# Performance work log

Hardware: AMD Instinct MI355X
Metric: run time of the kernel (lower is better)

## Reference

```python
import jax, jax.numpy as jnp
import numpy as np

B, E, T = 8192, 512, 32


def setup_inputs() -> dict:
    key = jax.random.key(0)
    k1, k2, k3, k4, k5, k6 = jax.random.split(key, 6)
    s1 = 1.0 / np.sqrt(E)  # torch nn.Linear default init scale (uniform bound)
    return {
        "g_exp": jax.random.normal(k1, (B, E), dtype=jnp.float32),
        "tissue_vector": jax.random.randint(k2, (B, 1), 0, T, dtype=jnp.int64),
        # per-tissue head params: Linear(E,E) then Linear(E,1)
        "W1": jax.random.uniform(k3, (T, E, E), jnp.float32, -s1, s1),
        "b1": jax.random.uniform(k4, (T, E), jnp.float32, -s1, s1),
        "W2": jax.random.uniform(k5, (T, E), jnp.float32, -s1, s1),
        "b2": jax.random.uniform(k6, (T,), jnp.float32, -s1, s1),
    }


def reference(g_exp, tissue_vector, W1, b1, W2, b2):
    # Each sample b is routed through the MLP head of its tissue id.
    # Vectorized: run every sample through every tissue head, then select.
    # h[b,t,:] = GELU(g_exp[b] @ W1[t] + b1[t])
    h = jax.nn.gelu(jnp.einsum("be,teh->bth", g_exp, W1) + b1[None, :, :],
                    approximate=False)  # exact erf GELU, matches torch nn.GELU
    # y[b,t] = softplus(h[b,t] @ W2[t] + b2[t])   (Softplus since loss_fn='poisson')
    y = jax.nn.softplus(jnp.einsum("bth,th->bt", h, W2) + b2[None, :])
    tid = tissue_vector[:, 0]  # [B], tissue id per sample
    return jnp.take_along_axis(y, tid[:, None], axis=1)  # [B, 1]
```

## Files before the change

### kernel.cpp

```cpp
#include <hip/hip_runtime.h>
#include <math.h>

#define B_N 8192
#define E_N 512
#define T_N 32
#define LDA 40

typedef short bf16x8 __attribute__((ext_vector_type(8)));
typedef float f32x4 __attribute__((ext_vector_type(4)));

#define WS_OFFS   256
#define WS_RANK   512
#define WS_ORDER  33280
#define WS_YACC   66048
#define WS_ASORT  98816
#define WS_W1T    8487424
#define WS_REQ    25264640

static __device__ __forceinline__ unsigned short f2bf(float f) {
    unsigned int u = __float_as_uint(f);
    unsigned int r = u + 0x7fffu + ((u >> 16) & 1u);
    return (unsigned short)(r >> 16);
}

__global__ __launch_bounds__(1024) void k_prep(
    const int* __restrict__ tv, int* __restrict__ offs_g,
    int* __restrict__ rank, int* __restrict__ order, float* __restrict__ yacc) {
    __shared__ int lh[16 * 32];
    __shared__ int wcur[16 * 32];
    __shared__ int offs_s[33];
    int tid = threadIdx.x;
    int w = tid >> 6;
    if (tid < 512) { lh[tid] = 0; }
    __syncthreads();
    int tval[8];
#pragma unroll
    for (int c = 0; c < 8; ++c) tval[c] = tv[c * 1024 + tid];
#pragma unroll
    for (int c = 0; c < 8; ++c) atomicAdd(&lh[w * 32 + tval[c]], 1);
    __syncthreads();
    if (tid < 32) {
        int s = 0;
#pragma unroll
        for (int ww = 0; ww < 16; ++ww) s += lh[ww * 32 + tid];
        int excl = 0;
#pragma unroll
        for (int i = 0; i < 32; ++i) {
            int v = __shfl(s, i, 64);
            if (i < tid) excl += v;
        }
        offs_s[tid] = excl;
        offs_g[tid] = excl;
        if (tid == 31) { offs_s[32] = excl + s; offs_g[32] = excl + s; }
    }
    __syncthreads();
    if (tid < 512) {
        int ww = tid >> 5, t = tid & 31;
        int s = offs_s[t];
        for (int w2 = 0; w2 < ww; ++w2) s += lh[w2 * 32 + t];
        wcur[ww * 32 + t] = s;
    }
    __syncthreads();
#pragma unroll
    for (int c = 0; c < 8; ++c) {
        int b = c * 1024 + tid;
        int pos = atomicAdd(&wcur[w * 32 + tval[c]], 1);
        rank[b] = pos;
        order[pos] = b;
    }
#pragma unroll
    for (int c = 0; c < 8; ++c) yacc[c * 1024 + tid] = 0.f;
}

__global__ __launch_bounds__(256) void k_convert(
    const float* __restrict__ W1, unsigned short* __restrict__ W1T,
    const float* __restrict__ g_exp, const int* __restrict__ rank,
    unsigned short* __restrict__ Asort) {
    int cid = blockIdx.x;
    int tid = threadIdx.x;
    if (cid < 2048) {
        __shared__ float T[64][65];
        int t = cid >> 6, r = cid & 63;
        int k0 = (r >> 3) * 64, n0 = (r & 7) * 64;
        int g = tid >> 4, c = tid & 15;
#pragma unroll
        for (int p = 0; p < 4; ++p) {
            int row = p * 16 + g;
            float4 v = *(const float4*)(W1 + ((size_t)t * E_N + k0 + row) * E_N + n0 + c * 4);
            T[c * 4 + 0][row] = v.x;
            T[c * 4 + 1][row] = v.y;
            T[c * 4 + 2][row] = v.z;
            T[c * 4 + 3][row] = v.w;
        }
        __syncthreads();
#pragma unroll
        for (int p = 0; p < 4; ++p) {
            int n = p * 16 + g;
            ushort4 o;
            o.x = f2bf(T[n][c * 4 + 0]);
            o.y = f2bf(T[n][c * 4 + 1]);
            o.z = f2bf(T[n][c * 4 + 2]);
            o.w = f2bf(T[n][c * 4 + 3]);
            *(ushort4*)(W1T + ((size_t)t * E_N + n0 + n) * E_N + k0 + c * 4) = o;
        }
    } else {
        int b0 = (cid - 2048) * 32;
#pragma unroll 4
        for (int pp = 0; pp < 16; ++pp) {
            int idx = pp * 256 + tid;
            int row = idx >> 7, c = idx & 127;
            int b = b0 + row;
            float4 v = *(const float4*)(g_exp + (size_t)b * E_N + c * 4);
            ushort4 o;
            o.x = f2bf(v.x); o.y = f2bf(v.y); o.z = f2bf(v.z); o.w = f2bf(v.w);
            *(ushort4*)(Asort + (size_t)rank[b] * E_N + c * 4) = o;
        }
    }
}

__global__ __launch_bounds__(256) void k_gemm_mfma(
    const unsigned short* __restrict__ Asort, const unsigned short* __restrict__ W1T,
    const float* __restrict__ b1, const float* __restrict__ W2,
    const int* __restrict__ offs, float* __restrict__ yacc) {
    int wi = blockIdx.x;
    int mt = wi >> 7;
    int rem = wi & 127;
    int t = rem >> 2, nt = rem & 3;
    int base = offs[t];
    int n_t = offs[t + 1] - base;
    int m0 = mt * 128;
    if (m0 >= n_t) return;
    int n0 = nt * 128;

    __shared__ __align__(16) unsigned short As[2][128 * LDA];
    __shared__ __align__(16) unsigned short Bs[2][128 * LDA];

    int tid = threadIdx.x;
    int wave = tid >> 6, lane = tid & 63;
    int quad = lane >> 4, l15 = lane & 15;
    int wm = (wave >> 1) * 64, wn = (wave & 1) * 64;

    int s_row0 = tid >> 2, s_c = tid & 3;
    int s_row1 = s_row0 + 64;
    int gr0 = base + m0 + s_row0; if (gr0 > B_N - 1) gr0 = B_N - 1;
    int gr1 = base + m0 + s_row1; if (gr1 > B_N - 1) gr1 = B_N - 1;
    const unsigned short* Bsrc = W1T + ((size_t)t * E_N + n0) * E_N;
    const unsigned short* a0p = Asort + (size_t)gr0 * E_N + s_c * 8;
    const unsigned short* a1p = Asort + (size_t)gr1 * E_N + s_c * 8;
    const unsigned short* b0p = Bsrc + (size_t)s_row0 * E_N + s_c * 8;
    const unsigned short* b1p = Bsrc + (size_t)s_row1 * E_N + s_c * 8;

    f32x4 acc[4][4];
#pragma unroll
    for (int mi = 0; mi < 4; ++mi)
#pragma unroll
        for (int ni = 0; ni < 4; ++ni) acc[mi][ni] = (f32x4){0.f, 0.f, 0.f, 0.f};

    int4 ar0, ar1, br0, br1;
    ar0 = *(const int4*)(a0p); ar1 = *(const int4*)(a1p);
    br0 = *(const int4*)(b0p); br1 = *(const int4*)(b1p);

    int buf = 0;
    for (int k0 = 0; k0 < E_N; k0 += 32) {
        *(int4*)(&As[buf][s_row0 * LDA + s_c * 8]) = ar0;
        *(int4*)(&As[buf][s_row1 * LDA + s_c * 8]) = ar1;
        *(int4*)(&Bs[buf][s_row0 * LDA + s_c * 8]) = br0;
        *(int4*)(&Bs[buf][s_row1 * LDA + s_c * 8]) = br1;
        if (k0 + 32 < E_N) {
            int koff = k0 + 32;
            ar0 = *(const int4*)(a0p + koff);
            ar1 = *(const int4*)(a1p + koff);
            br0 = *(const int4*)(b0p + koff);
            br1 = *(const int4*)(b1p + koff);
        }
        __syncthreads();
        bf16x8 af[4], bfr[4];
#pragma unroll
        for (int i = 0; i < 4; ++i) {
            af[i]  = *(const bf16x8*)(&As[buf][(wm + i * 16 + l15) * LDA + quad * 8]);
            bfr[i] = *(const bf16x8*)(&Bs[buf][(wn + i * 16 + l15) * LDA + quad * 8]);
        }
#pragma unroll
        for (int mi = 0; mi < 4; ++mi)
#pragma unroll
            for (int ni = 0; ni < 4; ++ni)
                acc[mi][ni] = __builtin_amdgcn_mfma_f32_16x16x32_bf16(
                    af[mi], bfr[ni], acc[mi][ni], 0, 0, 0);
        buf ^= 1;
    }

    float pr[4][4];
#pragma unroll
    for (int mi = 0; mi < 4; ++mi)
#pragma unroll
        for (int r = 0; r < 4; ++r) pr[mi][r] = 0.f;
#pragma unroll
    for (int ni = 0; ni < 4; ++ni) {
        int n = n0 + wn + ni * 16 + l15;
        float bb = b1[t * E_N + n];
        float w2 = W2[t * E_N + n];
#pragma unroll
        for (int mi = 0; mi < 4; ++mi)
#pragma unroll
            for (int r = 0; r < 4; ++r) {
                float u = acc[mi][ni][r] + bb;
                float gg = 0.5f * u * (1.f + erff(u * 0.70710678118654752f));
                pr[mi][r] = fmaf(gg, w2, pr[mi][r]);
            }
    }
#pragma unroll
    for (int off = 1; off <= 8; off <<= 1)
#pragma unroll
        for (int mi = 0; mi < 4; ++mi)
#pragma unroll
            for (int r = 0; r < 4; ++r) pr[mi][r] += __shfl_xor(pr[mi][r], off, 64);

    if (l15 == 0) {
#pragma unroll
        for (int mi = 0; mi < 4; ++mi)
#pragma unroll
            for (int r = 0; r < 4; ++r) {
                int row = m0 + wm + mi * 16 + quad * 4 + r;
                if (row < n_t) atomicAdd(&yacc[base + row], pr[mi][r]);
            }
    }
}

__global__ void k_final(const float* __restrict__ yacc, const int* __restrict__ rank,
                        const int* __restrict__ tv, const float* __restrict__ b2,
                        float* __restrict__ out, int use_rank) {
    int b = blockIdx.x * blockDim.x + threadIdx.x;
    if (b < B_N) {
        int idx = use_rank ? rank[b] : b;
        float x = yacc[idx] + b2[tv[b]];
        out[b] = fmaxf(x, 0.f) + log1pf(expf(-fabsf(x)));
    }
}

__global__ __launch_bounds__(256) void fb_gemm(
    const float* __restrict__ g_exp, const float* __restrict__ W1,
    const float* __restrict__ b1, const float* __restrict__ W2,
    const int* __restrict__ offs, const int* __restrict__ order,
    float* __restrict__ yacc) {
    int t = blockIdx.z;
    int base = offs[t];
    int n_t = offs[t + 1] - base;
    int m0 = blockIdx.y * 64;
    if (m0 >= n_t) return;
    int n0 = blockIdx.x * 128;

    __shared__ float As[32][68];
    __shared__ float Bs[32][128];
    __shared__ int sidx[64];

    int tid = threadIdx.x;
    if (tid < 64) {
        int m = m0 + tid;
        sidx[tid] = (m < n_t) ? order[base + m] : -1;
    }
    __syncthreads();

    int ty = tid >> 4, tx = tid & 15;
    float acc[4][8];
#pragma unroll
    for (int r = 0; r < 4; ++r)
#pragma unroll
        for (int c = 0; c < 8; ++c) acc[r][c] = 0.f;

    for (int k0 = 0; k0 < E_N; k0 += 32) {
#pragma unroll
        for (int p = 0; p < 2; ++p) {
            int idx = tid + 256 * p;
            int row = idx >> 3, kc = idx & 7;
            int s = sidx[row];
            float4 v = make_float4(0.f, 0.f, 0.f, 0.f);
            if (s >= 0) v = *(const float4*)(g_exp + (size_t)s * E_N + k0 + kc * 4);
            As[kc * 4 + 0][row] = v.x;
            As[kc * 4 + 1][row] = v.y;
            As[kc * 4 + 2][row] = v.z;
            As[kc * 4 + 3][row] = v.w;
        }
#pragma unroll
        for (int p = 0; p < 4; ++p) {
            int idx = tid + 256 * p;
            int kr = idx >> 5, c4 = idx & 31;
            *(float4*)(&Bs[kr][c4 * 4]) =
                *(const float4*)(W1 + ((size_t)t * E_N + (k0 + kr)) * E_N + n0 + c4 * 4);
        }
        __syncthreads();
#pragma unroll
        for (int e = 0; e < 32; ++e) {
            float4 a = *(const float4*)(&As[e][ty * 4]);
            float4 bA = *(const float4*)(&Bs[e][tx * 4]);
            float4 bB = *(const float4*)(&Bs[e][tx * 4 + 64]);
            float av[4] = {a.x, a.y, a.z, a.w};
            float bv[8] = {bA.x, bA.y, bA.z, bA.w, bB.x, bB.y, bB.z, bB.w};
#pragma unroll
            for (int r = 0; r < 4; ++r)
#pragma unroll
                for (int c = 0; c < 8; ++c) acc[r][c] = fmaf(av[r], bv[c], acc[r][c]);
        }
        __syncthreads();
    }

    float pr[4] = {0.f, 0.f, 0.f, 0.f};
#pragma unroll
    for (int c = 0; c < 8; ++c) {
        int n = n0 + tx * 4 + ((c >= 4) ? 64 : 0) + (c & 3);
        float bb = b1[t * E_N + n];
        float w2 = W2[t * E_N + n];
#pragma unroll
        for (int r = 0; r < 4; ++r) {
            float u = acc[r][c] + bb;
            float g = 0.5f * u * (1.f + erff(u * 0.70710678118654752f));
            pr[r] = fmaf(g, w2, pr[r]);
        }
    }
#pragma unroll
    for (int off = 8; off >= 1; off >>= 1)
#pragma unroll
        for (int r = 0; r < 4; ++r) pr[r] += __shfl_xor(pr[r], off, 64);

    if (tx == 0) {
#pragma unroll
        for (int r = 0; r < 4; ++r) {
            int m = m0 + ty * 4 + r;
            if (m < n_t) atomicAdd(&yacc[sidx[ty * 4 + r]], pr[r]);
        }
    }
}

extern "C" void kernel_launch(void* const* d_in, const int* in_sizes, int n_in,
                              void* d_out, int out_size, void* d_ws, size_t ws_size,
                              hipStream_t stream) {
    const float* g_exp = (const float*)d_in[0];
    const int*   tv    = (const int*)d_in[1];
    const float* W1    = (const float*)d_in[2];
    const float* b1    = (const float*)d_in[3];
    const float* W2    = (const float*)d_in[4];
    const float* b2    = (const float*)d_in[5];
    float* out = (float*)d_out;

    char* ws = (char*)d_ws;
    int* offs   = (int*)(ws + WS_OFFS);
    int* rank   = (int*)(ws + WS_RANK);
    int* order  = (int*)(ws + WS_ORDER);
    float* yacc = (float*)(ws + WS_YACC);

    if (ws_size >= (size_t)WS_REQ) {
        unsigned short* Asort = (unsigned short*)(ws + WS_ASORT);
        unsigned short* W1T   = (unsigned short*)(ws + WS_W1T);
        k_prep<<<1, 1024, 0, stream>>>(tv, offs, rank, order, yacc);
        k_convert<<<2304, 256, 0, stream>>>(W1, W1T, g_exp, rank, Asort);
        k_gemm_mfma<<<512, 256, 0, stream>>>(Asort, W1T, b1, W2, offs, yacc);
        k_final<<<32, 256, 0, stream>>>(yacc, rank, tv, b2, out, 1);
    } else {
        k_prep<<<1, 1024, 0, stream>>>(tv, offs, rank, order, yacc);
        fb_gemm<<<dim3(4, 8, 32), 256, 0, stream>>>(g_exp, W1, b1, W2, offs, order, yacc);
        k_final<<<32, 256, 0, stream>>>(yacc, rank, tv, b2, out, 0);
    }
}
```

Baseline: 137.2 us.

## Fuse tissue sort into W1 conversion and gather fp32 activations inside GEMM

The sort/histogram kernel is merged into the W1 transpose-convert kernel as one extra block, and the separate sorted bf16 activation buffer is removed. The GEMM now gathers fp32 rows of g_exp through the order array and converts them to bf16 in registers before writing to LDS. The B tile is loaded with global_load_lds direct-to-LDS copies using an unpadded stride. This removes one launch and one activation round trip through memory, at the cost of a single-block sort running alongside the conversion, possible LDS bank conflicts on the unpadded B tile, and conversion work inside the GEMM loop.

Result: slower. 144.8 us (+5.5%).

```diff
diff --git a/kernel.cpp b/kernel.cpp
--- a/kernel.cpp
+++ b/kernel.cpp
@@ -5,6 +5,7 @@
 #define E_N 512
 #define T_N 32
 #define LDA 40
+#define LDB 32
 
 typedef short bf16x8 __attribute__((ext_vector_type(8)));
 typedef float f32x4 __attribute__((ext_vector_type(4)));
@@ -13,71 +14,26 @@
 #define WS_RANK   512
 #define WS_ORDER  33280
 #define WS_YACC   66048
-#define WS_ASORT  98816
-#define WS_W1T    8487424
-#define WS_REQ    25264640
+#define WS_W1T    98816
+#define WS_REQ    (WS_W1T + (size_t)T_N * E_N * E_N * 2)
+
+typedef __attribute__((address_space(1))) const unsigned int gas_u32;
+typedef __attribute__((address_space(3))) unsigned int las_u32;
 
 static __device__ __forceinline__ unsigned short f2bf(float f) {
     unsigned int u = __float_as_uint(f);
     unsigned int r = u + 0x7fffu + ((u >> 16) & 1u);
     return (unsigned short)(r >> 16);
 }
-
-__global__ __launch_bounds__(1024) void k_prep(
+static __device__ __forceinline__ unsigned int pack2(float a, float b) {
+    return (unsigned int)f2bf(a) | ((unsigned int)f2bf(b) << 16);
+}
+
+__global__ __launch_bounds__(256) void k_pre(
+    const float* __restrict__ W1, unsigned short* __restrict__ W1T,
     const int* __restrict__ tv, int* __restrict__ offs_g,
     int* __restrict__ rank, int* __restrict__ order, float* __restrict__ yacc) {
-    __shared__ int lh[16 * 32];
-    __shared__ int wcur[16 * 32];
-    __shared__ int offs_s[33];
-    int tid = threadIdx.x;
-    int w = tid >> 6;
-    if (tid < 512) { lh[tid] = 0; }
-    __syncthreads();
-    int tval[8];
-#pragma unroll
-    for (int c = 0; c < 8; ++c) tval[c] = tv[c * 1024 + tid];
-#pragma unroll
-    for (int c = 0; c < 8; ++c) atomicAdd(&lh[w * 32 + tval[c]], 1);
-    __syncthreads();
-    if (tid < 32) {
-        int s = 0;
-#pragma unroll
-        for (int ww = 0; ww < 16; ++ww) s += lh[ww * 32 + tid];
-        int excl = 0;
-#pragma unroll
-        for (int i = 0; i < 32; ++i) {
-            int v = __shfl(s, i, 64);
-            if (i < tid) excl += v;
-        }
-        offs_s[tid] = excl;
-        offs_g[tid] = excl;
-        if (tid == 31) { offs_s[32] = excl + s; offs_g[32] = excl + s; }
-    }
-    __syncthreads();
-    if (tid < 512) {
-        int ww = tid >> 5, t = tid & 31;
-        int s = offs_s[t];
-        for (int w2 = 0; w2 < ww; ++w2) s += lh[w2 * 32 + t];
-        wcur[ww * 32 + t] = s;
-    }
-    __syncthreads();
-#pragma unroll
-    for (int c = 0; c < 8; ++c) {
-        int b = c * 1024 + tid;
-        int pos = atomicAdd(&wcur[w * 32 + tval[c]], 1);
-        rank[b] = pos;
-        order[pos] = b;
-    }
-#pragma unroll
-    for (int c = 0; c < 8; ++c) yacc[c * 1024 + tid] = 0.f;
-}
-
-__global__ __launch_bounds__(256) void k_convert(
-    const float* __restrict__ W1, unsigned short* __restrict__ W1T,
-    const float* __restrict__ g_exp, const int* __restrict__ rank,
-    unsigned short* __restrict__ Asort) {
-    int cid = blockIdx.x;
-    int tid = threadIdx.x;
+    int cid = blockIdx.x, tid = threadIdx.x;
     if (cid < 2048) {
         __shared__ float T[64][65];
         int t = cid >> 6, r = cid & 63;
@@ -104,24 +60,54 @@
             *(ushort4*)(W1T + ((size_t)t * E_N + n0 + n) * E_N + k0 + c * 4) = o;
         }
     } else {
-        int b0 = (cid - 2048) * 32;
-#pragma unroll 4
-        for (int pp = 0; pp < 16; ++pp) {
-            int idx = pp * 256 + tid;
-            int row = idx >> 7, c = idx & 127;
-            int b = b0 + row;
-            float4 v = *(const float4*)(g_exp + (size_t)b * E_N + c * 4);
-            ushort4 o;
-            o.x = f2bf(v.x); o.y = f2bf(v.y); o.z = f2bf(v.z); o.w = f2bf(v.w);
-            *(ushort4*)(Asort + (size_t)rank[b] * E_N + c * 4) = o;
-        }
+        __shared__ int lh[4][32], wcur[4][32], offs_s[33];
+        int w = tid >> 6;
+        if (tid < 128) lh[tid >> 5][tid & 31] = 0;
+        __syncthreads();
+        int tval[32];
+#pragma unroll
+        for (int c = 0; c < 32; ++c) tval[c] = tv[c * 256 + tid];
+#pragma unroll
+        for (int c = 0; c < 32; ++c) atomicAdd(&lh[w][tval[c]], 1);
+        __syncthreads();
+        if (tid < 32) {
+            int s = lh[0][tid] + lh[1][tid] + lh[2][tid] + lh[3][tid];
+            int excl = 0;
+#pragma unroll
+            for (int i = 0; i < 32; ++i) {
+                int v = __shfl(s, i, 64);
+                if (i < tid) excl += v;
+            }
+            offs_s[tid] = excl;
+            offs_g[tid] = excl;
+            if (tid == 31) { offs_s[32] = excl + s; offs_g[32] = excl + s; }
+        }
+        __syncthreads();
+        if (tid < 128) {
+            int ww = tid >> 5, t = tid & 31;
+            int s = offs_s[t];
+            for (int w2 = 0; w2 < ww; ++w2) s += lh[w2][t];
+            wcur[ww][t] = s;
+        }
+        __syncthreads();
+#pragma unroll
+        for (int c = 0; c < 32; ++c) {
+            int b = c * 256 + tid;
+            int pos = atomicAdd(&wcur[w][tval[c]], 1);
+            rank[b] = pos;
+            order[pos] = b;
+        }
+        float4 z = make_float4(0.f, 0.f, 0.f, 0.f);
+#pragma unroll
+        for (int c = 0; c < 8; ++c) *(float4*)(yacc + (c * 256 + tid) * 4) = z;
     }
 }
 
 __global__ __launch_bounds__(256) void k_gemm_mfma(
-    const unsigned short* __restrict__ Asort, const unsigned short* __restrict__ W1T,
+    const float* __restrict__ g_exp, const unsigned short* __restrict__ W1T,
     const float* __restrict__ b1, const float* __restrict__ W2,
-    const int* __restrict__ offs, float* __restrict__ yacc) {
+    const int* __restrict__ offs, const int* __restrict__ order,
+    float* __restrict__ yacc) {
     int wi = blockIdx.x;
     int mt = wi >> 7;
     int rem = wi & 127;
@@ -133,7 +119,7 @@
     int n0 = nt * 128;
 
     __shared__ __align__(16) unsigned short As[2][128 * LDA];
-    __shared__ __align__(16) unsigned short Bs[2][128 * LDA];
+    __shared__ __align__(16) unsigned short Bs[2][128 * LDB];
 
     int tid = threadIdx.x;
     int wave = tid >> 6, lane = tid & 63;
@@ -141,14 +127,12 @@
     int wm = (wave >> 1) * 64, wn = (wave & 1) * 64;
 
     int s_row0 = tid >> 2, s_c = tid & 3;
-    int s_row1 = s_row0 + 64;
-    int gr0 = base + m0 + s_row0; if (gr0 > B_N - 1) gr0 = B_N - 1;
-    int gr1 = base + m0 + s_row1; if (gr1 > B_N - 1) gr1 = B_N - 1;
+    int i0 = base + m0 + s_row0;       if (i0 > B_N - 1) i0 = B_N - 1;
+    int i1 = base + m0 + s_row0 + 64;  if (i1 > B_N - 1) i1 = B_N - 1;
+    int sidx0 = order[i0], sidx1 = order[i1];
+    const float* a0p = g_exp + (size_t)sidx0 * E_N + s_c * 8;
+    const float* a1p = g_exp + (size_t)sidx1 * E_N + s_c * 8;
     const unsigned short* Bsrc = W1T + ((size_t)t * E_N + n0) * E_N;
-    const unsigned short* a0p = Asort + (size_t)gr0 * E_N + s_c * 8;
-    const unsigned short* a1p = Asort + (size_t)gr1 * E_N + s_c * 8;
-    const unsigned short* b0p = Bsrc + (size_t)s_row0 * E_N + s_c * 8;
-    const unsigned short* b1p = Bsrc + (size_t)s_row1 * E_N + s_c * 8;
 
     f32x4 acc[4][4];
 #pragma unroll
@@ -156,29 +140,44 @@
 #pragma unroll
         for (int ni = 0; ni < 4; ++ni) acc[mi][ni] = (f32x4){0.f, 0.f, 0.f, 0.f};
 
-    int4 ar0, ar1, br0, br1;
-    ar0 = *(const int4*)(a0p); ar1 = *(const int4*)(a1p);
-    br0 = *(const int4*)(b0p); br1 = *(const int4*)(b1p);
+#pragma unroll
+    for (int p = 0; p < 2; ++p) {
+        int idx = p * 256 + tid;
+        const unsigned short* gp = Bsrc + (size_t)(idx >> 2) * E_N + (idx & 3) * 8;
+        __builtin_amdgcn_global_load_lds((gas_u32*)gp, (las_u32*)&Bs[0][idx * 8], 16, 0, 0);
+    }
+    {
+        float4 q0 = *(const float4*)(a0p), q1 = *(const float4*)(a0p + 4);
+        float4 q2 = *(const float4*)(a1p), q3 = *(const float4*)(a1p + 4);
+        uint4 w0 = {pack2(q0.x, q0.y), pack2(q0.z, q0.w), pack2(q1.x, q1.y), pack2(q1.z, q1.w)};
+        uint4 w1 = {pack2(q2.x, q2.y), pack2(q2.z, q2.w), pack2(q3.x, q3.y), pack2(q3.z, q3.w)};
+        *(uint4*)(&As[0][s_row0 * LDA + s_c * 8]) = w0;
+        *(uint4*)(&As[0][(s_row0 + 64) * LDA + s_c * 8]) = w1;
+    }
 
     int buf = 0;
-    for (int k0 = 0; k0 < E_N; k0 += 32) {
-        *(int4*)(&As[buf][s_row0 * LDA + s_c * 8]) = ar0;
-        *(int4*)(&As[buf][s_row1 * LDA + s_c * 8]) = ar1;
-        *(int4*)(&Bs[buf][s_row0 * LDA + s_c * 8]) = br0;
-        *(int4*)(&Bs[buf][s_row1 * LDA + s_c * 8]) = br1;
-        if (k0 + 32 < E_N) {
-            int koff = k0 + 32;
-            ar0 = *(const int4*)(a0p + koff);
-            ar1 = *(const int4*)(a1p + koff);
-            br0 = *(const int4*)(b0p + koff);
-            br1 = *(const int4*)(b1p + koff);
-        }
-        __syncthreads();
+    for (int it = 0; it < 16; ++it) {
+        __syncthreads();
+        bool pre = (it + 1 < 16);
+        float4 q0, q1, q2, q3;
+        if (pre) {
+            int k0n = (it + 1) * 32;
+#pragma unroll
+            for (int p = 0; p < 2; ++p) {
+                int idx = p * 256 + tid;
+                const unsigned short* gp = Bsrc + (size_t)(idx >> 2) * E_N + k0n + (idx & 3) * 8;
+                __builtin_amdgcn_global_load_lds((gas_u32*)gp, (las_u32*)&Bs[buf ^ 1][idx * 8], 16, 0, 0);
+            }
+            q0 = *(const float4*)(a0p + k0n);
+            q1 = *(const float4*)(a0p + k0n + 4);
+            q2 = *(const float4*)(a1p + k0n);
+            q3 = *(const float4*)(a1p + k0n + 4);
+        }
         bf16x8 af[4], bfr[4];
 #pragma unroll
         for (int i = 0; i < 4; ++i) {
             af[i]  = *(const bf16x8*)(&As[buf][(wm + i * 16 + l15) * LDA + quad * 8]);
-            bfr[i] = *(const bf16x8*)(&Bs[buf][(wn + i * 16 + l15) * LDA + quad * 8]);
+            bfr[i] = *(const bf16x8*)(&Bs[buf][(wn + i * 16 + l15) * LDB + quad * 8]);
         }
 #pragma unroll
         for (int mi = 0; mi < 4; ++mi)
@@ -186,6 +185,12 @@
             for (int ni = 0; ni < 4; ++ni)
                 acc[mi][ni] = __builtin_amdgcn_mfma_f32_16x16x32_bf16(
                     af[mi], bfr[ni], acc[mi][ni], 0, 0, 0);
+        if (pre) {
+            uint4 w0 = {pack2(q0.x, q0.y), pack2(q0.z, q0.w), pack2(q1.x, q1.y), pack2(q1.z, q1.w)};
+            uint4 w1 = {pack2(q2.x, q2.y), pack2(q2.z, q2.w), pack2(q3.x, q3.y), pack2(q3.z, q3.w)};
+            *(uint4*)(&As[buf ^ 1][s_row0 * LDA + s_c * 8]) = w0;
+            *(uint4*)(&As[buf ^ 1][(s_row0 + 64) * LDA + s_c * 8]) = w1;
+        }
         buf ^= 1;
     }
 
@@ -235,6 +240,51 @@
         float x = yacc[idx] + b2[tv[b]];
         out[b] = fmaxf(x, 0.f) + log1pf(expf(-fabsf(x)));
     }
+}
+
+__global__ __launch_bounds__(256) void k_prep_sb(
+    const int* __restrict__ tv, int* __restrict__ offs_g,
+    int* __restrict__ rank, int* __restrict__ order, float* __restrict__ yacc) {
+    __shared__ int lh[4][32], wcur[4][32], offs_s[33];
+    int tid = threadIdx.x, w = tid >> 6;
+    if (tid < 128) lh[tid >> 5][tid & 31] = 0;
+    __syncthreads();
+    int tval[32];
+#pragma unroll
+    for (int c = 0; c < 32; ++c) tval[c] = tv[c * 256 + tid];
+#pragma unroll
+    for (int c = 0; c < 32; ++c) atomicAdd(&lh[w][tval[c]], 1);
+    __syncthreads();
+    if (tid < 32) {
+        int s = lh[0][tid] + lh[1][tid] + lh[2][tid] + lh[3][tid];
+        int excl = 0;
+#pragma unroll
+        for (int i = 0; i < 32; ++i) {
+            int v = __shfl(s, i, 64);
+            if (i < tid) excl += v;
+        }
+        offs_s[tid] = excl;
+        offs_g[tid] = excl;
+        if (tid == 31) { offs_s[32] = excl + s; offs_g[32] = excl + s; }
+    }
+    __syncthreads();
+    if (tid < 128) {
+        int ww = tid >> 5, t = tid & 31;
+        int s = offs_s[t];
+        for (int w2 = 0; w2 < ww; ++w2) s += lh[w2][t];
+        wcur[ww][t] = s;
+    }
+    __syncthreads();
+#pragma unroll
+    for (int c = 0; c < 32; ++c) {
+        int b = c * 256 + tid;
+        int pos = atomicAdd(&wcur[w][tval[c]], 1);
+        rank[b] = pos;
+        order[pos] = b;
+    }
+    float4 z = make_float4(0.f, 0.f, 0.f, 0.f);
+#pragma unroll
+    for (int c = 0; c < 8; ++c) *(float4*)(yacc + (c * 256 + tid) * 4) = z;
 }
 
 __global__ __launch_bounds__(256) void fb_gemm(
@@ -347,15 +397,13 @@
     int* order  = (int*)(ws + WS_ORDER);
     float* yacc = (float*)(ws + WS_YACC);
 
-    if (ws_size >= (size_t)WS_REQ) {
-        unsigned short* Asort = (unsigned short*)(ws + WS_ASORT);
-        unsigned short* W1T   = (unsigned short*)(ws + WS_W1T);
-        k_prep<<<1, 1024, 0, stream>>>(tv, offs, rank, order, yacc);
-        k_convert<<<2304, 256, 0, stream>>>(W1, W1T, g_exp, rank, Asort);
-        k_gemm_mfma<<<512, 256, 0, stream>>>(Asort, W1T, b1, W2, offs, yacc);
+    if (ws_size >= WS_REQ) {
+        unsigned short* W1T = (unsigned short*)(ws + WS_W1T);
+        k_pre<<<2049, 256, 0, stream>>>(W1, W1T, tv, offs, rank, order, yacc);
+        k_gemm_mfma<<<512, 256, 0, stream>>>(g_exp, W1T, b1, W2, offs, order, yacc);
         k_final<<<32, 256, 0, stream>>>(yacc, rank, tv, b2, out, 1);
     } else {
-        k_prep<<<1, 1024, 0, stream>>>(tv, offs, rank, order, yacc);
+        k_prep_sb<<<1, 256, 0, stream>>>(tv, offs, rank, order, yacc);
         fb_gemm<<<dim3(4, 8, 32), 256, 0, stream>>>(g_exp, W1, b1, W2, offs, order, yacc);
         k_final<<<32, 256, 0, stream>>>(yacc, rank, tv, b2, out, 0);
     }
```
